# Performance work log

Hardware: AMD Instinct MI355X
Metric: run time of the kernel (lower is better)

Reference implementation:

```python
import jax, jax.numpy as jnp
import numpy as np

EMBED_DIM = 1024
NUM_HEADS = 16
HEAD_DIM = EMBED_DIM // NUM_HEADS


def setup_inputs() -> dict:
    key = jax.random.key(0)
    ks = jax.random.split(key, 9)
    B, S, D = 2, 2048, EMBED_DIM
    scale = 1.0 / np.sqrt(D)
    x = jax.random.normal(ks[0], (B, S, D), dtype=jnp.float32)
    Wq = jax.random.normal(ks[1], (D, D), dtype=jnp.float32) * scale
    Wk = jax.random.normal(ks[2], (D, D), dtype=jnp.float32) * scale
    Wv = jax.random.normal(ks[3], (D, D), dtype=jnp.float32) * scale
    Wo = jax.random.normal(ks[4], (D, D), dtype=jnp.float32) * scale
    bq = jnp.zeros((D,), jnp.float32)
    bk = jnp.zeros((D,), jnp.float32)
    bv = jnp.zeros((D,), jnp.float32)
    bo = jnp.zeros((D,), jnp.float32)
    return {"x": x, "Wq": Wq, "bq": bq, "Wk": Wk, "bk": bk,
            "Wv": Wv, "bv": bv, "Wo": Wo, "bo": bo}


def reference(x, Wq, bq, Wk, bk, Wv, bv, Wo, bo):
    B, S, D = x.shape
    H, Dh = NUM_HEADS, HEAD_DIM
    # QKV projections -> [B, H, S, Dh]
    q = (x @ Wq + bq).reshape(B, S, H, Dh).transpose(0, 2, 1, 3)
    k = (x @ Wk + bk).reshape(B, S, H, Dh).transpose(0, 2, 1, 3)
    v = (x @ Wv + bv).reshape(B, S, H, Dh).transpose(0, 2, 1, 3)
    # scores [B, H, S, S], scaled by sqrt(head_dim)
    scores = jnp.einsum('bhqd,bhkd->bhqk', q, k) / jnp.sqrt(jnp.float32(Dh))
    attn = jax.nn.softmax(scores, axis=-1)
    out = jnp.einsum('bhqk,bhkd->bhqd', attn, v)  # [B, H, S, Dh]
    out = out.transpose(0, 2, 1, 3).reshape(B, S, D)
    return out @ Wo + bo
```

## Files before the change

### kernel.cpp

```cpp
#include <hip/hip_runtime.h>
#include <hip/hip_bf16.h>

typedef short bf16x8 __attribute__((ext_vector_type(8)));
typedef float f32x4 __attribute__((ext_vector_type(4)));

#define MFMA16(a, b, c) __builtin_amdgcn_mfma_f32_16x16x32_bf16((a), (b), (c), 0, 0, 0)

static constexpr int B_ = 2, S_ = 2048, D_ = 1024, H_ = 16, DH = 64;
static constexpr int M_ = B_ * S_;
static constexpr int K_ = D_;

static __device__ __forceinline__ ushort f2bf(float f) {
    __hip_bfloat16 h = __float2bfloat16(f);
    return *reinterpret_cast<ushort*>(&h);
}

static __device__ __forceinline__ void gload16(const ushort* g, ushort* l) {
    __builtin_amdgcn_global_load_lds((const __attribute__((address_space(1))) void*)g,
                                     (__attribute__((address_space(3))) void*)l, 16, 0, 0);
}

__global__ __launch_bounds__(256) void cvt_f2b(const float* __restrict__ in,
                                               ushort* __restrict__ out) {
    int i = blockIdx.x * blockDim.x + threadIdx.x;
    float4 v = reinterpret_cast<const float4*>(in)[i];
    ushort4 o;
    o.x = f2bf(v.x); o.y = f2bf(v.y); o.z = f2bf(v.z); o.w = f2bf(v.w);
    reinterpret_cast<ushort4*>(out)[i] = o;
}

__global__ __launch_bounds__(256) void transpose_w4(const float* __restrict__ W0,
                                                    const float* __restrict__ W1,
                                                    const float* __restrict__ W2,
                                                    const float* __restrict__ W3,
                                                    ushort* __restrict__ T0,
                                                    ushort* __restrict__ T1,
                                                    ushort* __restrict__ T2,
                                                    ushort* __restrict__ T3) {
    __shared__ float tile[32][33];
    int z = blockIdx.z;
    const float* W = (z == 0) ? W0 : (z == 1) ? W1 : (z == 2) ? W2 : W3;
    ushort* T = (z == 0) ? T0 : (z == 1) ? T1 : (z == 2) ? T2 : T3;
    int bx = blockIdx.x, by = blockIdx.y;
    int tx = threadIdx.x, ty = threadIdx.y;
#pragma unroll
    for (int i = 0; i < 4; i++)
        tile[ty + i * 8][tx] = W[(by * 32 + ty + i * 8) * D_ + bx * 32 + tx];
    __syncthreads();
#pragma unroll
    for (int i = 0; i < 4; i++)
        T[(bx * 32 + ty + i * 8) * K_ + by * 32 + tx] = f2bf(tile[tx][ty + i * 8]);
}

template <int MODE>
__global__ __launch_bounds__(256, 2) void gemm128(const ushort* __restrict__ A,
                                                  const ushort* __restrict__ Wt,
                                                  const float* __restrict__ bias_q,
                                                  const float* __restrict__ bias_k,
                                                  const float* __restrict__ bias_v,
                                                  ushort* __restrict__ Qb,
                                                  ushort* __restrict__ Kb,
                                                  ushort* __restrict__ Vtb,
                                                  float* __restrict__ outf) {
    __shared__ __align__(16) ushort As[128 * 32];
    __shared__ __align__(16) ushort Bs[128 * 32];

    int m0 = blockIdx.x * 128;
    int n0 = blockIdx.y * 128;
    int t = threadIdx.x;
    int lane = t & 63, w = t >> 6;
    int ln = lane & 15, lq = lane >> 4;
    int wm = (w >> 1) * 64, wn = (w & 1) * 64;

    int c0 = t, c1 = t + 256;
    const ushort* Ag0 = A + (size_t)(m0 + (c0 >> 2)) * K_ + (c0 & 3) * 8;
    const ushort* Ag1 = A + (size_t)(m0 + (c1 >> 2)) * K_ + (c1 & 3) * 8;
    const ushort* Bg0 = Wt + (size_t)(n0 + (c0 >> 2)) * K_ + (c0 & 3) * 8;
    const ushort* Bg1 = Wt + (size_t)(n0 + (c1 >> 2)) * K_ + (c1 & 3) * 8;
    ushort* Al0 = As + c0 * 8;
    ushort* Al1 = As + c1 * 8;
    ushort* Bl0 = Bs + c0 * 8;
    ushort* Bl1 = Bs + c1 * 8;

    f32x4 acc[4][4];
#pragma unroll
    for (int i = 0; i < 4; i++)
#pragma unroll
        for (int j = 0; j < 4; j++) acc[i][j] = f32x4{0.f, 0.f, 0.f, 0.f};

    for (int k0 = 0; k0 < K_; k0 += 32) {
        gload16(Ag0 + k0, Al0);
        gload16(Ag1 + k0, Al1);
        gload16(Bg0 + k0, Bl0);
        gload16(Bg1 + k0, Bl1);
        __syncthreads();
        bf16x8 af[4], bfr[4];
#pragma unroll
        for (int i = 0; i < 4; i++)
            af[i] = *reinterpret_cast<const bf16x8*>(As + (wm + i * 16 + ln) * 32 + lq * 8);
#pragma unroll
        for (int j = 0; j < 4; j++)
            bfr[j] = *reinterpret_cast<const bf16x8*>(Bs + (wn + j * 16 + ln) * 32 + lq * 8);
#pragma unroll
        for (int i = 0; i < 4; i++)
#pragma unroll
            for (int j = 0; j < 4; j++)
                acc[i][j] = MFMA16(af[i], bfr[j], acc[i][j]);
        __syncthreads();
    }

#pragma unroll
    for (int j = 0; j < 4; j++) {
        int n = n0 + wn + j * 16 + ln;
        if (MODE == 1) {
            float bv = bias_q[n];
#pragma unroll
            for (int i = 0; i < 4; i++) {
#pragma unroll
                for (int r = 0; r < 4; r++) {
                    int m = m0 + wm + i * 16 + lq * 4 + r;
                    outf[(size_t)m * D_ + n] = acc[i][j][r] + bv;
                }
            }
        } else {
            int which = n >> 10, nn = n & 1023, h = nn >> 6, dh = nn & 63;
            const float* bp = (which == 0) ? bias_q : (which == 1) ? bias_k : bias_v;
            float bv = bp[nn];
            if (which == 2) {
#pragma unroll
                for (int i = 0; i < 4; i++) {
                    int m = m0 + wm + i * 16 + lq * 4;
                    int b = m >> 11, s0 = m & 2047;
                    ushort4 o4;
                    o4.x = f2bf(acc[i][j][0] + bv);
                    o4.y = f2bf(acc[i][j][1] + bv);
                    o4.z = f2bf(acc[i][j][2] + bv);
                    o4.w = f2bf(acc[i][j][3] + bv);
                    *reinterpret_cast<ushort4*>(Vtb + (((size_t)(b * H_ + h) * DH) + dh) * S_ + s0) = o4;
                }
            } else {
                ushort* dst = (which == 0) ? Qb : Kb;
#pragma unroll
                for (int i = 0; i < 4; i++) {
#pragma unroll
                    for (int r = 0; r < 4; r++) {
                        int m = m0 + wm + i * 16 + lq * 4 + r;
                        int b = m >> 11, s = m & 2047;
                        dst[(((b * H_ + h) * S_) + s) * DH + dh] = f2bf(acc[i][j][r] + bv);
                    }
                }
            }
        }
    }
}

__global__ __launch_bounds__(256, 2) void attn128(const ushort* __restrict__ Q,
                                                  const ushort* __restrict__ K,
                                                  const ushort* __restrict__ Vt,
                                                  ushort* __restrict__ O) {
    __shared__ __align__(16) ushort Kl[2][4096];
    __shared__ __align__(16) ushort Vl[2][4096];
    __shared__ __align__(16) ushort Pl[4][2][16 * 72];

    int bid = blockIdx.x;
    int qb = bid & 15;
    int bh = bid >> 4;
    int t = threadIdx.x;
    int lane = t & 63, w = t >> 6;
    int ln = lane & 15, lq = lane >> 4;

    const ushort* Qp = Q + (size_t)bh * S_ * DH;
    const ushort* Kp = K + (size_t)bh * S_ * DH;
    const ushort* Vp = Vt + (size_t)bh * DH * S_;

    int q0 = qb * 128 + w * 32;
    bf16x8 qf[2][2];
#pragma unroll
    for (int tl = 0; tl < 2; tl++) {
        const ushort* qp = Qp + (q0 + tl * 16 + ln) * DH + lq * 8;
        qf[tl][0] = *reinterpret_cast<const bf16x8*>(qp);
        qf[tl][1] = *reinterpret_cast<const bf16x8*>(qp + 32);
    }

    int c0 = t, c1 = t + 256;
    const ushort* Kg0 = Kp + (size_t)(c0 & 63) * DH + (c0 >> 6) * 8;
    const ushort* Kg1 = Kp + (size_t)(c1 & 63) * DH + (c1 >> 6) * 8;
    const ushort* Vg0 = Vp + (size_t)(c0 & 63) * S_ + (c0 >> 6) * 8;
    const ushort* Vg1 = Vp + (size_t)(c1 & 63) * S_ + (c1 >> 6) * 8;

    f32x4 o_acc[2][4];
    float l_part[2][4];
#pragma unroll
    for (int tl = 0; tl < 2; tl++)
#pragma unroll
        for (int nt = 0; nt < 4; nt++) {
            o_acc[tl][nt] = f32x4{0.f, 0.f, 0.f, 0.f};
            l_part[tl][nt] = 0.f;
        }

    gload16(Kg0, Kl[0] + c0 * 8);
    gload16(Kg1, Kl[0] + c1 * 8);
    gload16(Vg0, Vl[0] + c0 * 8);
    gload16(Vg1, Vl[0] + c1 * 8);

    const float kSc = 0.18033688011112042f;

    for (int kt = 0; kt < S_ / 64; kt++) {
        __syncthreads();
        int cur = kt & 1;
        if (kt + 1 < S_ / 64) {
            int kb = (kt + 1) * 64;
            gload16(Kg0 + (size_t)kb * DH, Kl[cur ^ 1] + c0 * 8);
            gload16(Kg1 + (size_t)kb * DH, Kl[cur ^ 1] + c1 * 8);
            gload16(Vg0 + kb, Vl[cur ^ 1] + c0 * 8);
            gload16(Vg1 + kb, Vl[cur ^ 1] + c1 * 8);
        }
        const ushort* Kc = Kl[cur];
        const ushort* Vc = Vl[cur];

        bf16x8 kf0[4], kf1[4];
#pragma unroll
        for (int nt = 0; nt < 4; nt++) {
            kf0[nt] = *reinterpret_cast<const bf16x8*>(Kc + (lq * 64 + nt * 16 + ln) * 8);
            kf1[nt] = *reinterpret_cast<const bf16x8*>(Kc + ((4 + lq) * 64 + nt * 16 + ln) * 8);
        }
        f32x4 sc[2][4];
#pragma unroll
        for (int tl = 0; tl < 2; tl++)
#pragma unroll
            for (int nt = 0; nt < 4; nt++) {
                f32x4 c = {0.f, 0.f, 0.f, 0.f};
                c = MFMA16(qf[tl][0], kf0[nt], c);
                c = MFMA16(qf[tl][1], kf1[nt], c);
                sc[tl][nt] = c;
            }
#pragma unroll
        for (int tl = 0; tl < 2; tl++)
#pragma unroll
            for (int nt = 0; nt < 4; nt++)
#pragma unroll
                for (int r = 0; r < 4; r++) {
                    float p = exp2f(sc[tl][nt][r] * kSc);
                    l_part[tl][r] += p;
                    Pl[w][tl][(lq * 4 + r) * 72 + nt * 16 + ln] = f2bf(p);
                }
        bf16x8 pf[2][2];
#pragma unroll
        for (int tl = 0; tl < 2; tl++) {
            pf[tl][0] = *reinterpret_cast<const bf16x8*>(&Pl[w][tl][ln * 72 + lq * 8]);
            pf[tl][1] = *reinterpret_cast<const bf16x8*>(&Pl[w][tl][ln * 72 + 32 + lq * 8]);
        }
#pragma unroll
        for (int nt = 0; nt < 4; nt++) {
            bf16x8 vf0 = *reinterpret_cast<const bf16x8*>(Vc + (lq * 64 + nt * 16 + ln) * 8);
            bf16x8 vf1 = *reinterpret_cast<const bf16x8*>(Vc + ((4 + lq) * 64 + nt * 16 + ln) * 8);
#pragma unroll
            for (int tl = 0; tl < 2; tl++) {
                o_acc[tl][nt] = MFMA16(pf[tl][0], vf0, o_acc[tl][nt]);
                o_acc[tl][nt] = MFMA16(pf[tl][1], vf1, o_acc[tl][nt]);
            }
        }
    }

    int b = bh >> 4, h = bh & 15;
#pragma unroll
    for (int tl = 0; tl < 2; tl++) {
        float linv[4];
#pragma unroll
        for (int r = 0; r < 4; r++) {
            float l = l_part[tl][r];
#pragma unroll
            for (int d = 1; d < 16; d <<= 1) l += __shfl_xor(l, d, 64);
            linv[r] = 1.0f / l;
        }
#pragma unroll
        for (int nt = 0; nt < 4; nt++)
#pragma unroll
            for (int r = 0; r < 4; r++) {
                int s = q0 + tl * 16 + lq * 4 + r;
                O[((b * S_ + s) * H_ + h) * DH + nt * 16 + ln] =
                    f2bf(o_acc[tl][nt][r] * linv[r]);
            }
    }
}

extern "C" void kernel_launch(void* const* d_in, const int* in_sizes, int n_in,
                              void* d_out, int out_size, void* d_ws, size_t ws_size,
                              hipStream_t stream) {
    const float* x  = (const float*)d_in[0];
    const float* Wq = (const float*)d_in[1];
    const float* bq = (const float*)d_in[2];
    const float* Wk = (const float*)d_in[3];
    const float* bk = (const float*)d_in[4];
    const float* Wv = (const float*)d_in[5];
    const float* bv = (const float*)d_in[6];
    const float* Wo = (const float*)d_in[7];
    const float* bo = (const float*)d_in[8];
    float* out = (float*)d_out;

    char* ws = (char*)d_ws;
    const size_t MB = 1024 * 1024;
    ushort* wtq = (ushort*)(ws + 0 * MB);
    ushort* wtk = (ushort*)(ws + 2 * MB);
    ushort* wtv = (ushort*)(ws + 4 * MB);
    ushort* wto = (ushort*)(ws + 6 * MB);
    ushort* xb  = (ushort*)(ws + 8 * MB);
    ushort* Qb  = (ushort*)(ws + 16 * MB);
    ushort* Kb  = (ushort*)(ws + 24 * MB);
    ushort* Vtb = (ushort*)(ws + 32 * MB);
    ushort* AO  = (ushort*)(ws + 40 * MB);

    cvt_f2b<<<(M_ * K_ / 4) / 256, 256, 0, stream>>>(x, xb);

    transpose_w4<<<dim3(32, 32, 4), dim3(32, 8), 0, stream>>>(
        Wq, Wk, Wv, Wo, wtq, wtk, wtv, wto);

    gemm128<0><<<dim3(M_ / 128, 3072 / 128), 256, 0, stream>>>(
        xb, wtq, bq, bk, bv, Qb, Kb, Vtb, nullptr);

    attn128<<<32 * 16, 256, 0, stream>>>(Qb, Kb, Vtb, AO);

    gemm128<1><<<dim3(M_ / 128, D_ / 128), 256, 0, stream>>>(
        AO, wto, bo, nullptr, nullptr, nullptr, nullptr, nullptr, out);
}
```

Before: 219.0 us.

## Halve attention query tile per block and raise GEMM occupancy hint

The attention kernel now gives each wave one 16-row query tile instead of two, so a block covers 64 queries and the grid doubles to 1024 blocks. This cuts per-thread registers and spreads work across more CUs, but each K/V tile is now loaded and read from LDS for half as many queries, which doubles K/V global and LDS traffic per query. The GEMM launch bound also rises to 4 blocks per SM, which pushes the compiler to use fewer registers and risks spills.

```diff
diff --git a/kernel.cpp b/kernel.cpp
--- a/kernel.cpp
+++ b/kernel.cpp
@@ -53,7 +53,7 @@
 }
 
 template <int MODE>
-__global__ __launch_bounds__(256, 2) void gemm128(const ushort* __restrict__ A,
+__global__ __launch_bounds__(256, 4) void gemm128(const ushort* __restrict__ A,
                                                   const ushort* __restrict__ Wt,
                                                   const float* __restrict__ bias_q,
                                                   const float* __restrict__ bias_k,
@@ -154,33 +154,28 @@
     }
 }
 
-__global__ __launch_bounds__(256, 2) void attn128(const ushort* __restrict__ Q,
-                                                  const ushort* __restrict__ K,
-                                                  const ushort* __restrict__ Vt,
-                                                  ushort* __restrict__ O) {
+__global__ __launch_bounds__(256) void attn64d(const ushort* __restrict__ Q,
+                                               const ushort* __restrict__ K,
+                                               const ushort* __restrict__ Vt,
+                                               ushort* __restrict__ O) {
     __shared__ __align__(16) ushort Kl[2][4096];
     __shared__ __align__(16) ushort Vl[2][4096];
-    __shared__ __align__(16) ushort Pl[4][2][16 * 72];
+    __shared__ __align__(16) short Pl[4][16 * 72];
 
     int bid = blockIdx.x;
-    int qb = bid & 15;
-    int bh = bid >> 4;
+    int qb = bid & 31;
+    int bh = bid >> 5;
     int t = threadIdx.x;
     int lane = t & 63, w = t >> 6;
     int ln = lane & 15, lq = lane >> 4;
+    int qt = qb * 4 + w;
 
     const ushort* Qp = Q + (size_t)bh * S_ * DH;
     const ushort* Kp = K + (size_t)bh * S_ * DH;
     const ushort* Vp = Vt + (size_t)bh * DH * S_;
 
-    int q0 = qb * 128 + w * 32;
-    bf16x8 qf[2][2];
-#pragma unroll
-    for (int tl = 0; tl < 2; tl++) {
-        const ushort* qp = Qp + (q0 + tl * 16 + ln) * DH + lq * 8;
-        qf[tl][0] = *reinterpret_cast<const bf16x8*>(qp);
-        qf[tl][1] = *reinterpret_cast<const bf16x8*>(qp + 32);
-    }
+    bf16x8 qf0 = *reinterpret_cast<const bf16x8*>(Qp + (qt * 16 + ln) * DH + lq * 8);
+    bf16x8 qf1 = *reinterpret_cast<const bf16x8*>(Qp + (qt * 16 + ln) * DH + 32 + lq * 8);
 
     int c0 = t, c1 = t + 256;
     const ushort* Kg0 = Kp + (size_t)(c0 & 63) * DH + (c0 >> 6) * 8;
@@ -188,15 +183,10 @@
     const ushort* Vg0 = Vp + (size_t)(c0 & 63) * S_ + (c0 >> 6) * 8;
     const ushort* Vg1 = Vp + (size_t)(c1 & 63) * S_ + (c1 >> 6) * 8;
 
-    f32x4 o_acc[2][4];
-    float l_part[2][4];
-#pragma unroll
-    for (int tl = 0; tl < 2; tl++)
-#pragma unroll
-        for (int nt = 0; nt < 4; nt++) {
-            o_acc[tl][nt] = f32x4{0.f, 0.f, 0.f, 0.f};
-            l_part[tl][nt] = 0.f;
-        }
+    f32x4 o_acc[4];
+    float l_part[4] = {0.f, 0.f, 0.f, 0.f};
+#pragma unroll
+    for (int nt = 0; nt < 4; nt++) o_acc[nt] = f32x4{0.f, 0.f, 0.f, 0.f};
 
     gload16(Kg0, Kl[0] + c0 * 8);
     gload16(Kg1, Kl[0] + c1 * 8);
@@ -218,70 +208,52 @@
         const ushort* Kc = Kl[cur];
         const ushort* Vc = Vl[cur];
 
-        bf16x8 kf0[4], kf1[4];
+        f32x4 sc[4];
 #pragma unroll
         for (int nt = 0; nt < 4; nt++) {
-            kf0[nt] = *reinterpret_cast<const bf16x8*>(Kc + (lq * 64 + nt * 16 + ln) * 8);
-            kf1[nt] = *reinterpret_cast<const bf16x8*>(Kc + ((4 + lq) * 64 + nt * 16 + ln) * 8);
-        }
-        f32x4 sc[2][4];
-#pragma unroll
-        for (int tl = 0; tl < 2; tl++)
-#pragma unroll
-            for (int nt = 0; nt < 4; nt++) {
-                f32x4 c = {0.f, 0.f, 0.f, 0.f};
-                c = MFMA16(qf[tl][0], kf0[nt], c);
-                c = MFMA16(qf[tl][1], kf1[nt], c);
-                sc[tl][nt] = c;
+            bf16x8 kf0 = *reinterpret_cast<const bf16x8*>(Kc + (lq * 64 + nt * 16 + ln) * 8);
+            bf16x8 kf1 = *reinterpret_cast<const bf16x8*>(Kc + ((4 + lq) * 64 + nt * 16 + ln) * 8);
+            f32x4 c = {0.f, 0.f, 0.f, 0.f};
+            c = MFMA16(qf0, kf0, c);
+            c = MFMA16(qf1, kf1, c);
+            sc[nt] = c;
+        }
+#pragma unroll
+        for (int nt = 0; nt < 4; nt++)
+#pragma unroll
+            for (int r = 0; r < 4; r++) {
+                float p = exp2f(sc[nt][r] * kSc);
+                l_part[r] += p;
+                Pl[w][(lq * 4 + r) * 72 + nt * 16 + ln] = (short)f2bf(p);
             }
-#pragma unroll
-        for (int tl = 0; tl < 2; tl++)
-#pragma unroll
-            for (int nt = 0; nt < 4; nt++)
-#pragma unroll
-                for (int r = 0; r < 4; r++) {
-                    float p = exp2f(sc[tl][nt][r] * kSc);
-                    l_part[tl][r] += p;
-                    Pl[w][tl][(lq * 4 + r) * 72 + nt * 16 + ln] = f2bf(p);
-                }
-        bf16x8 pf[2][2];
-#pragma unroll
-        for (int tl = 0; tl < 2; tl++) {
-            pf[tl][0] = *reinterpret_cast<const bf16x8*>(&Pl[w][tl][ln * 72 + lq * 8]);
-            pf[tl][1] = *reinterpret_cast<const bf16x8*>(&Pl[w][tl][ln * 72 + 32 + lq * 8]);
-        }
+        bf16x8 pf0 = *reinterpret_cast<const bf16x8*>(&Pl[w][ln * 72 + lq * 8]);
+        bf16x8 pf1 = *reinterpret_cast<const bf16x8*>(&Pl[w][ln * 72 + 32 + lq * 8]);
 #pragma unroll
         for (int nt = 0; nt < 4; nt++) {
             bf16x8 vf0 = *reinterpret_cast<const bf16x8*>(Vc + (lq * 64 + nt * 16 + ln) * 8);
             bf16x8 vf1 = *reinterpret_cast<const bf16x8*>(Vc + ((4 + lq) * 64 + nt * 16 + ln) * 8);
-#pragma unroll
-            for (int tl = 0; tl < 2; tl++) {
-                o_acc[tl][nt] = MFMA16(pf[tl][0], vf0, o_acc[tl][nt]);
-                o_acc[tl][nt] = MFMA16(pf[tl][1], vf1, o_acc[tl][nt]);
-            }
-        }
-    }
-
+            o_acc[nt] = MFMA16(pf0, vf0, o_acc[nt]);
+            o_acc[nt] = MFMA16(pf1, vf1, o_acc[nt]);
+        }
+    }
+
+    float linv[4];
+#pragma unroll
+    for (int r = 0; r < 4; r++) {
+        float l = l_part[r];
+#pragma unroll
+        for (int d = 1; d < 16; d <<= 1) l += __shfl_xor(l, d, 64);
+        linv[r] = 1.0f / l;
+    }
     int b = bh >> 4, h = bh & 15;
 #pragma unroll
-    for (int tl = 0; tl < 2; tl++) {
-        float linv[4];
+    for (int nt = 0; nt < 4; nt++)
 #pragma unroll
         for (int r = 0; r < 4; r++) {
-            float l = l_part[tl][r];
-#pragma unroll
-            for (int d = 1; d < 16; d <<= 1) l += __shfl_xor(l, d, 64);
-            linv[r] = 1.0f / l;
-        }
-#pragma unroll
-        for (int nt = 0; nt < 4; nt++)
-#pragma unroll
-            for (int r = 0; r < 4; r++) {
-                int s = q0 + tl * 16 + lq * 4 + r;
-                O[((b * S_ + s) * H_ + h) * DH + nt * 16 + ln] =
-                    f2bf(o_acc[tl][nt][r] * linv[r]);
-            }
-    }
+            int s = qt * 16 + lq * 4 + r;
+            O[((b * S_ + s) * H_ + h) * DH + nt * 16 + ln] =
+                f2bf(o_acc[nt][r] * linv[r]);
+        }
 }
 
 extern "C" void kernel_launch(void* const* d_in, const int* in_sizes, int n_in,
@@ -318,7 +290,7 @@
     gemm128<0><<<dim3(M_ / 128, 3072 / 128), 256, 0, stream>>>(
         xb, wtq, bq, bk, bv, Qb, Kb, Vtb, nullptr);
 
-    attn128<<<32 * 16, 256, 0, stream>>>(Qb, Kb, Vtb, AO);
+    attn64d<<<32 * 32, 256, 0, stream>>>(Qb, Kb, Vtb, AO);
 
     gemm128<1><<<dim3(M_ / 128, D_ / 128), 256, 0, stream>>>(
         AO, wto, bo, nullptr, nullptr, nullptr, nullptr, nullptr, out);
```

After: 240.9 us. +10.0%, slower.
